# Kernel optimization log

Hardware: AMD Instinct MI355X
Metric: run time of the kernel (lower is better)

Reference implementation:

```python
import jax, jax.numpy as jnp
import numpy as np

B, V, T = 512, 50257, 2048   # batch, vocab, history length
TOP_K = 50                    # from __init__ arg top_k
NEG_INF = jnp.float32(-1e30)  # finite stand-in for -inf (same softmax result, clean grads)


def setup_inputs() -> dict:
    key = jax.random.key(0)
    k1, k2, k3 = jax.random.split(key, 3)
    logits = jax.random.normal(k1, (B, V), jnp.float32) * 4.0
    previous_tokens = jax.random.randint(k2, (B, T), 0, V)
    # uniform noise for the Gumbel-max trick (torch.rand_like); avoid log(0)
    rand_u = jax.random.uniform(k3, (B, V), jnp.float32, minval=1e-10, maxval=1.0)
    return {
        "logits": logits,
        "previous_tokens": previous_tokens,
        "rand_u": rand_u,
        "temperature": jnp.full((1, 1), 0.8, jnp.float32),
        "top_p": jnp.full((1, 1), 0.8, jnp.float32),
        "repetition_penalty": jnp.full((1, 1), 1.35, jnp.float32),
    }


def _logits_to_probs(logits, previous_tokens, temperature, top_p, repetition_penalty):
    b = jnp.arange(logits.shape[0])[:, None]
    # repetition penalty: gather scores at previous tokens, rescale, scatter back
    score = jnp.take_along_axis(logits, previous_tokens, axis=1)            # [B, T]
    score = jnp.where(score < 0, score * repetition_penalty, score / repetition_penalty)
    logits = logits.at[b, previous_tokens].set(score)
    # top-p (nucleus) filtering: sort descending, cumulative softmax mass
    order = jnp.argsort(-logits, axis=-1)                                   # [B, V]
    sorted_logits = jnp.take_along_axis(logits, order, axis=1)
    cum_probs = jnp.cumsum(jax.nn.softmax(sorted_logits, axis=-1), axis=-1)
    remove_sorted = cum_probs > top_p
    remove_sorted = remove_sorted.at[:, 0].set(False)                       # always keep best token
    # unsort the removal mask back to vocab order (order is a permutation)
    remove = jnp.zeros_like(remove_sorted).at[b, order].set(remove_sorted)
    logits = jnp.where(remove, NEG_INF, logits)
    # temperature
    logits = logits / jnp.maximum(temperature, 1e-5)
    # top-k filtering: mask everything below the k-th largest logit
    v = jax.lax.top_k(logits, TOP_K)[0]                                     # [B, TOP_K]
    pivot = v[:, -1:]
    logits = jnp.where(logits < pivot, NEG_INF, logits)
    return jax.nn.softmax(logits, axis=-1)


def reference(logits, previous_tokens, rand_u, temperature, top_p, repetition_penalty):
    probs = _logits_to_probs(logits, previous_tokens, temperature, top_p, repetition_penalty)
    # Gumbel-max multinomial sample: argmax(probs / Exp(1))
    q = -jnp.log(rand_u)
    idx_next = jnp.argmax(probs / q, axis=-1, keepdims=True).astype(jnp.int64)
    return idx_next, probs
```

## Files before the change

kernel.cpp:

```cpp
#include <hip/hip_runtime.h>
#include <cstdint>
#include <cmath>

#define V_SIZE 50257
#define T_SIZE 2048
#define B_SIZE 512
#define CAND_MAX 1024
#define SPEC_THRESH 10.0f
#define SPEC_MIN 80
#define KOFF 32.0f

#define NTHR1 1024
#define NWAVE1 (NTHR1 / 64)
#define NTHR2 512
#define NWAVE2 (NTHR2 / 64)

#define BM_WORDS ((V_SIZE + 31) / 32)

#define SCR_BASE (V_SIZE - (2 * CAND_MAX + 2))
#define SCR_VALS (SCR_BASE)
#define SCR_IDX  (SCR_BASE + CAND_MAX)
#define SCR_CNT  (SCR_BASE + 2 * CAND_MAX)
#define SCR_STOT (SCR_BASE + 2 * CAND_MAX + 1)

extern "C" __global__ __launch_bounds__(NTHR1, 8)
void pass1_kernel(const float* __restrict__ logits,
                  const int*   __restrict__ prev,
                  const float* __restrict__ repp,
                  float* __restrict__ out)
{
    const int row  = blockIdx.x;
    const int tid  = threadIdx.x;
    const int lane = tid & 63;
    const int wid  = tid >> 6;

    __shared__ unsigned int bitmap[BM_WORDS];
    __shared__ float cval[CAND_MAX];
    __shared__ int   cidx[CAND_MAX];
    __shared__ float redf[NWAVE1];
    __shared__ int   sCnt;

    const float rp = repp[0];
    const float* lrow = logits + (size_t)row * V_SIZE;
    float*       orow = out + B_SIZE + (size_t)row * V_SIZE;

    for (int i = tid; i < BM_WORDS; i += NTHR1) bitmap[i] = 0u;
    if (tid == 0) sCnt = 0;
    __syncthreads();

    const int* prow = prev + (size_t)row * T_SIZE;
    float corr = 0.0f;
    for (int i = tid; i < T_SIZE; i += NTHR1) {
        int v = prow[i];
        unsigned bit = 1u << (v & 31);
        unsigned old = atomicOr(&bitmap[((unsigned)v) >> 5], bit);
        if (!(old & bit)) {
            float x  = lrow[v];
            float xp = (x < 0.0f) ? x * rp : x / rp;
            corr += __expf(xp - KOFF) - __expf(x - KOFF);
        }
    }

    const int head  = (4 - (row & 3)) & 3;
    const int nvec  = (V_SIZE - head) >> 2;
    const int tails = head + nvec * 4;
    const float4* lrow4 = (const float4*)(lrow + head);

    float lz0 = 0.0f, lz1 = 0.0f;
    auto collect = [&](float x, int v) {
        if (x > SPEC_THRESH) {
            int p = atomicAdd(&sCnt, 1);
            if (p < CAND_MAX) { cval[p] = x; cidx[p] = v; }
        }
    };
    if (tid < head) {
        float x = lrow[tid];
        collect(x, tid);
        lz0 += __expf(x - KOFF);
    }
    if (tid < V_SIZE - tails) {
        float x = lrow[tails + tid];
        collect(x, tails + tid);
        lz0 += __expf(x - KOFF);
    }
    for (int i = tid; i < nvec; i += NTHR1) {
        float4 x4 = lrow4[i];
        int v = head + i * 4;
        collect(x4.x, v);     collect(x4.y, v + 1);
        collect(x4.z, v + 2); collect(x4.w, v + 3);
        lz0 += __expf(x4.x - KOFF) + __expf(x4.z - KOFF);
        lz1 += __expf(x4.y - KOFF) + __expf(x4.w - KOFF);
    }
    __syncthreads();

    const int C = min(sCnt, CAND_MAX);
    for (int i = tid; i < C; i += NTHR1) {
        int v = cidx[i];
        if ((bitmap[((unsigned)v) >> 5] >> (v & 31)) & 1u) {
            float x = cval[i];
            cval[i] = (x < 0.0f) ? x * rp : x / rp;
        }
    }

    float wz = lz0 + lz1 + corr;
    for (int off = 32; off; off >>= 1) wz += __shfl_down(wz, off);
    if (lane == 0) redf[wid] = wz;
    __syncthreads();

    for (int i = tid; i < C; i += NTHR1) {
        orow[SCR_VALS + i] = cval[i];
        orow[SCR_IDX  + i] = __int_as_float(cidx[i]);
    }
    if (tid == 0) {
        float s = 0.0f;
        for (int i = 0; i < NWAVE1; ++i) s += redf[i];
        orow[SCR_CNT]  = __int_as_float(sCnt);
        orow[SCR_STOT] = s;
    }
}

extern "C" __global__ __launch_bounds__(NTHR2, 8)
void decide_kernel(const float* __restrict__ logits,
                   const int*   __restrict__ prev,
                   const float* __restrict__ rand_u,
                   const float* __restrict__ tempp,
                   const float* __restrict__ toppp,
                   const float* __restrict__ repp,
                   float* __restrict__ out)
{
    const int row  = blockIdx.x;
    const int tid  = threadIdx.x;
    const int lane = tid & 63;
    const int wid  = tid >> 6;

    __shared__ unsigned int bitmap[BM_WORDS];
    __shared__ float cval[CAND_MAX];
    __shared__ int   cidx[CAND_MAX];
    __shared__ float rbuf[CAND_MAX];
    __shared__ float redf[NWAVE2];
    __shared__ int   redi[NWAVE2];
    __shared__ float sM, sZ, sS;
    __shared__ int   sCnt, sSend;

    const float rp   = repp[0];
    const float topp = toppp[0];
    const float temp = fmaxf(tempp[0], 1e-5f);

    const size_t rowoff = (size_t)row * V_SIZE;
    const float* lrow = logits + rowoff;
    const float* urow = rand_u + rowoff;
    float*       orow = out + B_SIZE + rowoff;

    const int   cntRaw = __float_as_int(orow[SCR_CNT]);
    const float stot   = orow[SCR_STOT];

    int C = 0;
    float M = 0.0f, Z = 1.0f;
    bool ok = (cntRaw >= SPEC_MIN && cntRaw <= CAND_MAX);

    if (ok) {
        C = cntRaw;
        float lm = -INFINITY;
        for (int i = tid; i < C; i += NTHR2) {
            float v = orow[SCR_VALS + i];
            cval[i] = v;
            cidx[i] = __float_as_int(orow[SCR_IDX + i]);
            lm = fmaxf(lm, v);
        }
        for (int off = 32; off; off >>= 1) lm = fmaxf(lm, __shfl_down(lm, off));
        if (lane == 0) redf[wid] = lm;
        __syncthreads();
        if (tid == 0) {
            float m = redf[0];
            for (int i = 1; i < NWAVE2; ++i) m = fmaxf(m, redf[i]);
            sM = m;
        }
        __syncthreads();
        M = sM;
        Z = stot * expf(KOFF - M);
        if (!(M > SPEC_THRESH)) ok = false;
    }

    if (!ok) {
        for (int i = tid; i < BM_WORDS; i += NTHR2) bitmap[i] = 0u;
        __syncthreads();
        const int* prow = prev + (size_t)row * T_SIZE;
        for (int i = tid; i < T_SIZE; i += NTHR2) {
            int v = prow[i];
            atomicOr(&bitmap[((unsigned)v) >> 5], 1u << (v & 31));
        }
        __syncthreads();

        float lm = -INFINITY, lz = 0.0f;
        for (int v = tid; v < V_SIZE; v += NTHR2) {
            float x = lrow[v];
            if ((bitmap[((unsigned)v) >> 5] >> (v & 31)) & 1u)
                x = (x < 0.0f) ? x * rp : x / rp;
            lm = fmaxf(lm, x);
            lz += __expf(x - KOFF);
        }
        {
            float wm = lm;
            for (int off = 32; off; off >>= 1) wm = fmaxf(wm, __shfl_down(wm, off));
            if (lane == 0) redf[wid] = wm;
        }
        __syncthreads();
        if (tid == 0) {
            float m = redf[0];
            for (int i = 1; i < NWAVE2; ++i) m = fmaxf(m, redf[i]);
            sM = m;
        }
        __syncthreads();
        M = sM;
        {
            float wz = lz;
            for (int off = 32; off; off >>= 1) wz += __shfl_down(wz, off);
            if (lane == 0) redf[wid] = wz;
        }
        __syncthreads();
        if (tid == 0) {
            float s = 0.0f;
            for (int i = 0; i < NWAVE2; ++i) s += redf[i];
            sZ = s * expf(KOFF - M);
        }
        __syncthreads();
        Z = sZ;

        auto count_pass = [&](float thr) -> int {
            __syncthreads();
            if (tid == 0) sCnt = 0;
            __syncthreads();
            int local = 0;
            for (int v = tid; v < V_SIZE; v += NTHR2) {
                float x = lrow[v];
                if ((bitmap[((unsigned)v) >> 5] >> (v & 31)) & 1u)
                    x = (x < 0.0f) ? x * rp : x / rp;
                if (x > thr) local++;
            }
            if (local) atomicAdd(&sCnt, local);
            __syncthreads();
            return sCnt;
        };
        float a = -200.0f, b = 200.0f, thr = 0.0f;
        int c = 0;
        for (int it = 0; it < 40; ++it) {
            thr = 0.5f * (a + b);
            c = count_pass(thr);
            if (c < SPEC_MIN)       b = thr;
            else if (c > CAND_MAX)  a = thr;
            else break;
        }
        if (c < SPEC_MIN) thr = a;
        __syncthreads();
        if (tid == 0) sCnt = 0;
        __syncthreads();
        for (int v = tid; v < V_SIZE; v += NTHR2) {
            float x = lrow[v];
            if ((bitmap[((unsigned)v) >> 5] >> (v & 31)) & 1u)
                x = (x < 0.0f) ? x * rp : x / rp;
            if (x > thr) {
                int p = atomicAdd(&sCnt, 1);
                if (p < CAND_MAX) { cval[p] = x; cidx[p] = v; }
            }
        }
        __syncthreads();
        C = min(sCnt, CAND_MAX);
    }

    for (int i = tid; i < 2 * CAND_MAX + 2; i += NTHR2)
        orow[SCR_BASE + i] = 0.0f;

    int n = 1; while (n < C) n <<= 1;
    for (int i = C + tid; i < n; i += NTHR2) { cval[i] = -INFINITY; cidx[i] = 0x7FFFFFFF; }
    __syncthreads();
    for (int k = 2; k <= n; k <<= 1) {
        for (int j = k >> 1; j > 0; j >>= 1) {
            for (int i = tid; i < n; i += NTHR2) {
                int l = i ^ j;
                if (l > i) {
                    float vi = cval[i], vl = cval[l];
                    int   ii = cidx[i], il = cidx[l];
                    bool lFirst = (vl > vi) || (vl == vi && il < ii);
                    bool asc = ((i & k) == 0);
                    if (lFirst == asc) {
                        cval[i] = vl; cval[l] = vi;
                        cidx[i] = il; cidx[l] = ii;
                    }
                }
            }
            __syncthreads();
        }
    }

    for (int i = tid; i < C; i += NTHR2)
        rbuf[i] = expf(cval[i] - M) / Z;
    __syncthreads();

    if (tid == 0) {
        float cum = 0.0f;
        int m = 0;
        float vp = cval[min(49, C - 1)];
        for (int i = 0; i < C; ++i) {
            cum += rbuf[i];
            if (i > 0 && cum > topp) break;
            m = i;
            if (m >= 49 && cval[i] < vp) break;
        }
        int send;
        if (m >= 49) {
            int e = 49;
            while (e + 1 < C && cval[e + 1] == vp) ++e;
            send = (m < e) ? m : e;
        } else {
            send = m;
        }
        sSend = send;
    }
    __syncthreads();

    const int send = sSend;
    const float v0 = cval[0];
    for (int i = tid; i <= send; i += NTHR2)
        rbuf[i] = expf(cval[i] / temp - v0 / temp);
    __syncthreads();
    if (tid == 0) {
        float S = 0.0f;
        for (int i = 0; i <= send; ++i) S += rbuf[i];
        sS = S;
    }
    __syncthreads();
    const float S = sS;

    float bestr = -1.0f;
    int   besti = 0x7FFFFFFF;
    for (int i = tid; i <= send; i += NTHR2) {
        float p = rbuf[i] / S;
        int v = cidx[i];
        orow[v] = p;
        float q = -logf(urow[v]);
        float r = p / q;
        if (r > bestr || (r == bestr && v < besti)) { bestr = r; besti = v; }
    }
    for (int off = 32; off; off >>= 1) {
        float r2 = __shfl_down(bestr, off);
        int   i2 = __shfl_down(besti, off);
        if (r2 > bestr || (r2 == bestr && i2 < besti)) { bestr = r2; besti = i2; }
    }
    if (lane == 0) { redf[wid] = bestr; redi[wid] = besti; }
    __syncthreads();
    if (tid == 0) {
        float br = redf[0]; int bi = redi[0];
        for (int i = 1; i < NWAVE2; ++i) {
            if (redf[i] > br || (redf[i] == br && redi[i] < bi)) { br = redf[i]; bi = redi[i]; }
        }
        out[row] = (float)bi;
    }
}

extern "C" void kernel_launch(void* const* d_in, const int* in_sizes, int n_in,
                              void* d_out, int out_size, void* d_ws, size_t ws_size,
                              hipStream_t stream) {
    const float* logits = (const float*)d_in[0];
    const int*   prev   = (const int*)d_in[1];
    const float* rand_u = (const float*)d_in[2];
    const float* tempp  = (const float*)d_in[3];
    const float* toppp  = (const float*)d_in[4];
    const float* repp   = (const float*)d_in[5];
    float* out = (float*)d_out;

    (void)hipMemsetAsync(d_out, 0, (size_t)out_size, stream);

    hipLaunchKernelGGL(pass1_kernel, dim3(B_SIZE), dim3(NTHR1), 0, stream,
                       logits, prev, repp, out);
    hipLaunchKernelGGL(decide_kernel, dim3(B_SIZE), dim3(NTHR2), 0, stream,
                       logits, prev, rand_u, tempp, toppp, repp, out);
}
```

Baseline: 255.6 us.

## Fuse candidate-collection and decision kernels; register/shuffle bitonic sort for small sets

Merges the two per-row kernels into one 1024-thread kernel, so candidates, bitmap and partition sum stay in shared memory instead of round-tripping through scratch space in the output buffer. This removes a kernel launch, the scratch writes, reads and zeroing, and the fallback path's bitmap rebuild. It also adds a bitonic sort variant for up to 512 candidates that keeps elements in registers and uses wave shuffles for strides under 64, syncing through shared memory only for larger strides. The trade-off is that the decision phase now runs at 1024 threads with more shared memory per block, which may reduce occupancy.

```diff
diff --git a/kernel.cpp b/kernel.cpp
--- a/kernel.cpp
+++ b/kernel.cpp
@@ -10,22 +10,17 @@
 #define SPEC_MIN 80
 #define KOFF 32.0f
 
-#define NTHR1 1024
-#define NWAVE1 (NTHR1 / 64)
-#define NTHR2 512
-#define NWAVE2 (NTHR2 / 64)
+#define NTHR 1024
+#define NWAVE (NTHR / 64)
 
 #define BM_WORDS ((V_SIZE + 31) / 32)
 
-#define SCR_BASE (V_SIZE - (2 * CAND_MAX + 2))
-#define SCR_VALS (SCR_BASE)
-#define SCR_IDX  (SCR_BASE + CAND_MAX)
-#define SCR_CNT  (SCR_BASE + 2 * CAND_MAX)
-#define SCR_STOT (SCR_BASE + 2 * CAND_MAX + 1)
-
-extern "C" __global__ __launch_bounds__(NTHR1, 8)
-void pass1_kernel(const float* __restrict__ logits,
+extern "C" __global__ __launch_bounds__(NTHR, 8)
+void fused_kernel(const float* __restrict__ logits,
                   const int*   __restrict__ prev,
+                  const float* __restrict__ rand_u,
+                  const float* __restrict__ tempp,
+                  const float* __restrict__ toppp,
                   const float* __restrict__ repp,
                   float* __restrict__ out)
 {
@@ -37,20 +32,29 @@
     __shared__ unsigned int bitmap[BM_WORDS];
     __shared__ float cval[CAND_MAX];
     __shared__ int   cidx[CAND_MAX];
-    __shared__ float redf[NWAVE1];
-    __shared__ int   sCnt;
-
-    const float rp = repp[0];
-    const float* lrow = logits + (size_t)row * V_SIZE;
-    float*       orow = out + B_SIZE + (size_t)row * V_SIZE;
-
-    for (int i = tid; i < BM_WORDS; i += NTHR1) bitmap[i] = 0u;
+    __shared__ float rbuf[CAND_MAX];
+    __shared__ float redf[NWAVE];
+    __shared__ float redm[NWAVE];
+    __shared__ int   redi[NWAVE];
+    __shared__ float sM, sZ, sS, sStot;
+    __shared__ int   sCnt, sSend;
+
+    const float rp   = repp[0];
+    const float topp = toppp[0];
+    const float temp = fmaxf(tempp[0], 1e-5f);
+
+    const size_t rowoff = (size_t)row * V_SIZE;
+    const float* lrow = logits + rowoff;
+    const float* urow = rand_u + rowoff;
+    float*       orow = out + B_SIZE + rowoff;
+
+    for (int i = tid; i < BM_WORDS; i += NTHR) bitmap[i] = 0u;
     if (tid == 0) sCnt = 0;
     __syncthreads();
 
     const int* prow = prev + (size_t)row * T_SIZE;
     float corr = 0.0f;
-    for (int i = tid; i < T_SIZE; i += NTHR1) {
+    for (int i = tid; i < T_SIZE; i += NTHR) {
         int v = prow[i];
         unsigned bit = 1u << (v & 31);
         unsigned old = atomicOr(&bitmap[((unsigned)v) >> 5], bit);
@@ -83,7 +87,7 @@
         collect(x, tails + tid);
         lz0 += __expf(x - KOFF);
     }
-    for (int i = tid; i < nvec; i += NTHR1) {
+    for (int i = tid; i < nvec; i += NTHR) {
         float4 x4 = lrow4[i];
         int v = head + i * 4;
         collect(x4.x, v);     collect(x4.y, v + 1);
@@ -93,106 +97,43 @@
     }
     __syncthreads();
 
-    const int C = min(sCnt, CAND_MAX);
-    for (int i = tid; i < C; i += NTHR1) {
+    const int Craw = sCnt;
+    int C = min(Craw, CAND_MAX);
+    for (int i = tid; i < C; i += NTHR) {
         int v = cidx[i];
         if ((bitmap[((unsigned)v) >> 5] >> (v & 31)) & 1u) {
             float x = cval[i];
             cval[i] = (x < 0.0f) ? x * rp : x / rp;
         }
     }
-
-    float wz = lz0 + lz1 + corr;
-    for (int off = 32; off; off >>= 1) wz += __shfl_down(wz, off);
-    if (lane == 0) redf[wid] = wz;
-    __syncthreads();
-
-    for (int i = tid; i < C; i += NTHR1) {
-        orow[SCR_VALS + i] = cval[i];
-        orow[SCR_IDX  + i] = __int_as_float(cidx[i]);
-    }
+    {
+        float wz = lz0 + lz1 + corr;
+        for (int off = 32; off; off >>= 1) wz += __shfl_down(wz, off);
+        if (lane == 0) redf[wid] = wz;
+    }
+    __syncthreads();
+
+    {
+        float lm = -INFINITY;
+        for (int i = tid; i < C; i += NTHR) lm = fmaxf(lm, cval[i]);
+        for (int off = 32; off; off >>= 1) lm = fmaxf(lm, __shfl_down(lm, off));
+        if (lane == 0) redm[wid] = lm;
+    }
+    __syncthreads();
     if (tid == 0) {
-        float s = 0.0f;
-        for (int i = 0; i < NWAVE1; ++i) s += redf[i];
-        orow[SCR_CNT]  = __int_as_float(sCnt);
-        orow[SCR_STOT] = s;
-    }
-}
-
-extern "C" __global__ __launch_bounds__(NTHR2, 8)
-void decide_kernel(const float* __restrict__ logits,
-                   const int*   __restrict__ prev,
-                   const float* __restrict__ rand_u,
-                   const float* __restrict__ tempp,
-                   const float* __restrict__ toppp,
-                   const float* __restrict__ repp,
-                   float* __restrict__ out)
-{
-    const int row  = blockIdx.x;
-    const int tid  = threadIdx.x;
-    const int lane = tid & 63;
-    const int wid  = tid >> 6;
-
-    __shared__ unsigned int bitmap[BM_WORDS];
-    __shared__ float cval[CAND_MAX];
-    __shared__ int   cidx[CAND_MAX];
-    __shared__ float rbuf[CAND_MAX];
-    __shared__ float redf[NWAVE2];
-    __shared__ int   redi[NWAVE2];
-    __shared__ float sM, sZ, sS;
-    __shared__ int   sCnt, sSend;
-
-    const float rp   = repp[0];
-    const float topp = toppp[0];
-    const float temp = fmaxf(tempp[0], 1e-5f);
-
-    const size_t rowoff = (size_t)row * V_SIZE;
-    const float* lrow = logits + rowoff;
-    const float* urow = rand_u + rowoff;
-    float*       orow = out + B_SIZE + rowoff;
-
-    const int   cntRaw = __float_as_int(orow[SCR_CNT]);
-    const float stot   = orow[SCR_STOT];
-
-    int C = 0;
-    float M = 0.0f, Z = 1.0f;
-    bool ok = (cntRaw >= SPEC_MIN && cntRaw <= CAND_MAX);
-
-    if (ok) {
-        C = cntRaw;
-        float lm = -INFINITY;
-        for (int i = tid; i < C; i += NTHR2) {
-            float v = orow[SCR_VALS + i];
-            cval[i] = v;
-            cidx[i] = __float_as_int(orow[SCR_IDX + i]);
-            lm = fmaxf(lm, v);
-        }
-        for (int off = 32; off; off >>= 1) lm = fmaxf(lm, __shfl_down(lm, off));
-        if (lane == 0) redf[wid] = lm;
-        __syncthreads();
-        if (tid == 0) {
-            float m = redf[0];
-            for (int i = 1; i < NWAVE2; ++i) m = fmaxf(m, redf[i]);
-            sM = m;
-        }
-        __syncthreads();
-        M = sM;
-        Z = stot * expf(KOFF - M);
-        if (!(M > SPEC_THRESH)) ok = false;
-    }
+        float s = 0.0f, m = -INFINITY;
+        for (int i = 0; i < NWAVE; ++i) { s += redf[i]; m = fmaxf(m, redm[i]); }
+        sStot = s; sM = m;
+    }
+    __syncthreads();
+
+    float M = sM;
+    float Z = sStot * expf(KOFF - M);
+    bool ok = (Craw >= SPEC_MIN && Craw <= CAND_MAX && M > SPEC_THRESH);
 
     if (!ok) {
-        for (int i = tid; i < BM_WORDS; i += NTHR2) bitmap[i] = 0u;
-        __syncthreads();
-        const int* prow = prev + (size_t)row * T_SIZE;
-        for (int i = tid; i < T_SIZE; i += NTHR2) {
-            int v = prow[i];
-            atomicOr(&bitmap[((unsigned)v) >> 5], 1u << (v & 31));
-        }
-        __syncthreads();
-
         float lm = -INFINITY, lz = 0.0f;
-        for (int v = tid; v < V_SIZE; v += NTHR2) {
+        for (int v = tid; v < V_SIZE; v += NTHR) {
             float x = lrow[v];
             if ((bitmap[((unsigned)v) >> 5] >> (v & 31)) & 1u)
                 x = (x < 0.0f) ? x * rp : x / rp;
@@ -202,12 +143,12 @@
         {
             float wm = lm;
             for (int off = 32; off; off >>= 1) wm = fmaxf(wm, __shfl_down(wm, off));
-            if (lane == 0) redf[wid] = wm;
+            if (lane == 0) redm[wid] = wm;
         }
         __syncthreads();
         if (tid == 0) {
-            float m = redf[0];
-            for (int i = 1; i < NWAVE2; ++i) m = fmaxf(m, redf[i]);
+            float m = redm[0];
+            for (int i = 1; i < NWAVE; ++i) m = fmaxf(m, redm[i]);
             sM = m;
         }
         __syncthreads();
@@ -220,7 +161,7 @@
         __syncthreads();
         if (tid == 0) {
             float s = 0.0f;
-            for (int i = 0; i < NWAVE2; ++i) s += redf[i];
+            for (int i = 0; i < NWAVE; ++i) s += redf[i];
             sZ = s * expf(KOFF - M);
         }
         __syncthreads();
@@ -231,7 +172,7 @@
             if (tid == 0) sCnt = 0;
             __syncthreads();
             int local = 0;
-            for (int v = tid; v < V_SIZE; v += NTHR2) {
+            for (int v = tid; v < V_SIZE; v += NTHR) {
                 float x = lrow[v];
                 if ((bitmap[((unsigned)v) >> 5] >> (v & 31)) & 1u)
                     x = (x < 0.0f) ? x * rp : x / rp;
@@ -254,7 +195,7 @@
         __syncthreads();
         if (tid == 0) sCnt = 0;
         __syncthreads();
-        for (int v = tid; v < V_SIZE; v += NTHR2) {
+        for (int v = tid; v < V_SIZE; v += NTHR) {
             float x = lrow[v];
             if ((bitmap[((unsigned)v) >> 5] >> (v & 31)) & 1u)
                 x = (x < 0.0f) ? x * rp : x / rp;
@@ -267,32 +208,62 @@
         C = min(sCnt, CAND_MAX);
     }
 
-    for (int i = tid; i < 2 * CAND_MAX + 2; i += NTHR2)
-        orow[SCR_BASE + i] = 0.0f;
-
     int n = 1; while (n < C) n <<= 1;
-    for (int i = C + tid; i < n; i += NTHR2) { cval[i] = -INFINITY; cidx[i] = 0x7FFFFFFF; }
-    __syncthreads();
-    for (int k = 2; k <= n; k <<= 1) {
-        for (int j = k >> 1; j > 0; j >>= 1) {
-            for (int i = tid; i < n; i += NTHR2) {
-                int l = i ^ j;
-                if (l > i) {
-                    float vi = cval[i], vl = cval[l];
-                    int   ii = cidx[i], il = cidx[l];
-                    bool lFirst = (vl > vi) || (vl == vi && il < ii);
-                    bool asc = ((i & k) == 0);
-                    if (lFirst == asc) {
-                        cval[i] = vl; cval[l] = vi;
-                        cidx[i] = il; cidx[l] = ii;
+    for (int i = C + tid; i < n; i += NTHR) { cval[i] = -INFINITY; cidx[i] = 0x7FFFFFFF; }
+    __syncthreads();
+
+    if (n <= 512) {
+        const int t = tid;
+        const bool act = (t < n);
+        float v = 0.0f; int id = 0;
+        if (act) { v = cval[t]; id = cidx[t]; }
+        for (int k = 2; k <= n; k <<= 1) {
+            for (int j = k >> 1; j > 0; j >>= 1) {
+                float pv = 0.0f; int pid = 0;
+                if (j >= 64) {
+                    __syncthreads();
+                    if (act) { cval[t] = v; cidx[t] = id; }
+                    __syncthreads();
+                    if (act) { pv = cval[t ^ j]; pid = cidx[t ^ j]; }
+                } else if (act) {
+                    pv  = __shfl_xor(v, j);
+                    pid = __shfl_xor(id, j);
+                }
+                if (act) {
+                    const bool amLow = ((t & j) == 0);
+                    const float vi = amLow ? v : pv,  vl = amLow ? pv : v;
+                    const int   ii = amLow ? id : pid, il = amLow ? pid : id;
+                    const bool lFirst = (vl > vi) || (vl == vi && il < ii);
+                    const bool asc = ((t & k) == 0);
+                    if (lFirst == asc) { v = pv; id = pid; }
+                }
+            }
+        }
+        __syncthreads();
+        if (act) { cval[t] = v; cidx[t] = id; }
+        __syncthreads();
+    } else {
+        for (int k = 2; k <= n; k <<= 1) {
+            for (int j = k >> 1; j > 0; j >>= 1) {
+                for (int i = tid; i < n; i += NTHR) {
+                    int l = i ^ j;
+                    if (l > i) {
+                        float vi = cval[i], vl = cval[l];
+                        int   ii = cidx[i], il = cidx[l];
+                        bool lFirst = (vl > vi) || (vl == vi && il < ii);
+                        bool asc = ((i & k) == 0);
+                        if (lFirst == asc) {
+                            cval[i] = vl; cval[l] = vi;
+                            cidx[i] = il; cidx[l] = ii;
+                        }
                     }
                 }
+                __syncthreads();
             }
-            __syncthreads();
-        }
-    }
-
-    for (int i = tid; i < C; i += NTHR2)
+        }
+    }
+
+    for (int i = tid; i < C; i += NTHR)
         rbuf[i] = expf(cval[i] - M) / Z;
     __syncthreads();
 
@@ -320,7 +291,7 @@
 
     const int send = sSend;
     const float v0 = cval[0];
-    for (int i = tid; i <= send; i += NTHR2)
+    for (int i = tid; i <= send; i += NTHR)
         rbuf[i] = expf(cval[i] / temp - v0 / temp);
     __syncthreads();
     if (tid == 0) {
@@ -333,7 +304,7 @@
 
     float bestr = -1.0f;
     int   besti = 0x7FFFFFFF;
-    for (int i = tid; i <= send; i += NTHR2) {
+    for (int i = tid; i <= send; i += NTHR) {
         float p = rbuf[i] / S;
         int v = cidx[i];
         orow[v] = p;
@@ -350,7 +321,7 @@
     __syncthreads();
     if (tid == 0) {
         float br = redf[0]; int bi = redi[0];
-        for (int i = 1; i < NWAVE2; ++i) {
+        for (int i = 1; i < NWAVE; ++i) {
             if (redf[i] > br || (redf[i] == br && redi[i] < bi)) { br = redf[i]; bi = redi[i]; }
         }
         out[row] = (float)bi;
@@ -370,8 +341,6 @@
 
     (void)hipMemsetAsync(d_out, 0, (size_t)out_size, stream);
 
-    hipLaunchKernelGGL(pass1_kernel, dim3(B_SIZE), dim3(NTHR1), 0, stream,
-                       logits, prev, repp, out);
-    hipLaunchKernelGGL(decide_kernel, dim3(B_SIZE), dim3(NTHR2), 0, stream,
+    hipLaunchKernelGGL(fused_kernel, dim3(B_SIZE), dim3(NTHR), 0, stream,
                        logits, prev, rand_u, tempp, toppp, repp, out);
 }
```

Measured after the change: 252.9 us. About the same (-1.1%).
